# Kernel optimization log

Hardware: AMD Instinct MI355X
Metric: run time of the kernel (lower is better)

Reference implementation:

```python
import jax, jax.numpy as jnp
import numpy as np

B, T, H, S = 2, 2048, 16, 64
EMB = H * S  # 1024


def layer_norm(x, g, b, eps=1e-5):
    mu = jnp.mean(x, axis=-1, keepdims=True)
    var = jnp.var(x, axis=-1, keepdims=True)
    return (x - mu) * jax.lax.rsqrt(var + eps) * g + b


def setup_inputs() -> dict:
    key = jax.random.key(0)
    ks = jax.random.split(key, 12)
    sc = 0.02
    return {
        "x": jax.random.normal(ks[0], (B, T, EMB), dtype=jnp.float32),
        "Wkqv": jax.random.normal(ks[1], (S, 3 * S), dtype=jnp.float32) * sc,
        "Wproj": jax.random.normal(ks[2], (EMB, EMB), dtype=jnp.float32) * sc,
        "g1": jnp.ones((EMB,), jnp.float32),
        "b1": jnp.zeros((EMB,), jnp.float32),
        "W1": jax.random.normal(ks[3], (EMB, 4 * EMB), dtype=jnp.float32) * sc,
        "bff1": jnp.zeros((4 * EMB,), jnp.float32),
        "W2": jax.random.normal(ks[4], (4 * EMB, EMB), dtype=jnp.float32) * sc,
        "bff2": jnp.zeros((EMB,), jnp.float32),
        "g2": jnp.ones((EMB,), jnp.float32),
        "b2": jnp.zeros((EMB,), jnp.float32),
    }


def reference(x, Wkqv, Wproj, g1, b1, W1, bff1, W2, bff2, g2, b2):
    Bb, Tt, _ = x.shape
    xh = x.reshape(Bb, Tt, H, S)                     # [B,T,H,S]
    kqv = jnp.einsum('bths,sd->bthd', xh, Wkqv)      # [B,T,H,3S], shared per-head weight
    k, q, v = jnp.split(kqv, 3, axis=-1)             # note order: k, q, v
    scores = jnp.einsum('bihk,bjhk->bijh', q, k) / jnp.sqrt(jnp.float32(S))
    att = jax.nn.softmax(scores, axis=2)             # softmax over key dim j
    res = jnp.einsum('btih,bihs->bths', att, v).reshape(Bb, Tt, EMB)
    mha = res @ Wproj                                # Linear(emb, emb, bias=False)
    x = layer_norm(x + mha, g1, b1)
    h = jax.nn.gelu(x @ W1 + bff1, approximate=False)
    ff = h @ W2 + bff2
    return layer_norm(x + ff, g2, b2)
```

## Files before the change

### kernel.cpp

```cpp
#include <hip/hip_runtime.h>
#include <hip/hip_bf16.h>
#include <math.h>

#define B_ 2
#define T_ 2048
#define H_ 16
#define S_ 64
#define EMB 1024
#define FF 4096
#define BT (B_*T_)
#define ROWS (B_*T_*H_)

typedef __attribute__((ext_vector_type(8))) short s16x8;
typedef __attribute__((ext_vector_type(4))) float f32x4;

struct P4 { unsigned short* p[4]; };

__device__ __forceinline__ unsigned short f2b(float f) {
    return __builtin_bit_cast(unsigned short, __float2bfloat16(f));
}
__device__ __forceinline__ float b2f(short u) {
    return __builtin_bit_cast(float, ((unsigned int)(unsigned short)u) << 16);
}

__device__ __forceinline__ void gl_lds16(const void* g, void* l) {
    __builtin_amdgcn_global_load_lds(
        (const __attribute__((address_space(1))) void*)g,
        (__attribute__((address_space(3))) void*)l, 16, 0, 0);
}

__device__ __forceinline__ f32x4 mfma16(s16x8 a, s16x8 b, f32x4 c) {
    return __builtin_amdgcn_mfma_f32_16x16x32_bf16(a, b, c, 0, 0, 0);
}

#define WAIT_VM8 0x0F78
#define WAIT_VM2 0x0F72
#define WAIT_VM0 0x0F70

__global__ __launch_bounds__(256) void kqv_kernel(const float* __restrict__ x,
        const unsigned short* __restrict__ Wqt, unsigned short* __restrict__ K,
        unsigned short* __restrict__ Q, unsigned short* __restrict__ V) {
    const int tid = threadIdx.x;
    const int w = tid >> 6, lane = tid & 63;
    const int l15 = lane & 15, quad = lane >> 4;
    const long r0 = (long)blockIdx.x * 128 + w * 32;

    s16x8 af[2][2];
    #pragma unroll
    for (int mt = 0; mt < 2; ++mt)
        #pragma unroll
        for (int ks = 0; ks < 2; ++ks) {
            const float* xp = x + (r0 + mt*16 + l15) * 64 + ks*32 + quad*8;
            const float4 v0 = *(const float4*)xp;
            const float4 v1 = *(const float4*)(xp + 4);
            s16x8 a;
            a[0] = (short)f2b(v0.x); a[1] = (short)f2b(v0.y);
            a[2] = (short)f2b(v0.z); a[3] = (short)f2b(v0.w);
            a[4] = (short)f2b(v1.x); a[5] = (short)f2b(v1.y);
            a[6] = (short)f2b(v1.z); a[7] = (short)f2b(v1.w);
            af[mt][ks] = a;
        }

    #pragma unroll
    for (int nt = 0; nt < 12; ++nt) {
        const s16x8 b0 = *(const s16x8*)&Wqt[(nt*16 + l15)*64 + quad*8];
        const s16x8 b1 = *(const s16x8*)&Wqt[(nt*16 + l15)*64 + 32 + quad*8];
        f32x4 acc[2] = {};
        #pragma unroll
        for (int mt = 0; mt < 2; ++mt) {
            acc[mt] = mfma16(af[mt][0], b0, acc[mt]);
            acc[mt] = mfma16(af[mt][1], b1, acc[mt]);
        }
        unsigned short* dst = (nt < 4) ? K : (nt < 8) ? Q : V;
        const int c0 = (nt & 3) * 16 + l15;
        #pragma unroll
        for (int mt = 0; mt < 2; ++mt)
            #pragma unroll
            for (int r = 0; r < 4; ++r)
                dst[(r0 + mt*16 + quad*4 + r) * 64 + c0] = f2b(acc[mt][r]);
    }
}

__global__ __launch_bounds__(256) void vt_kernel(const unsigned short* __restrict__ V,
        unsigned short* __restrict__ VT) {
    __shared__ unsigned short Ts[64][72];
    const int tid = threadIdx.x;
    const int tt = blockIdx.x, bh = blockIdx.y;
    const int b = bh >> 4, h = bh & 15;
    const long vbase = ((long)b * (T_*H_) + h) * 64;
    #pragma unroll
    for (int i = 0; i < 2; ++i) {
        const int id = i * 256 + tid;
        const int tr = id >> 3, dc = (id & 7) * 8;
        const s16x8 v = *(const s16x8*)&V[vbase + (long)(tt*64 + tr)*1024 + dc];
        *(s16x8*)&Ts[tr][dc] = v;
    }
    __syncthreads();
    #pragma unroll
    for (int i = 0; i < 2; ++i) {
        const int id = i * 256 + tid;
        const int d = id >> 3, tc = (id & 7) * 8;
        s16x8 o;
        #pragma unroll
        for (int j = 0; j < 8; ++j) o[j] = (short)Ts[tc + j][d];
        *(s16x8*)&VT[((long)bh*64 + d)*2048 + tt*64 + tc] = o;
    }
}

__global__ __launch_bounds__(256) void attn_kernel(const unsigned short* __restrict__ Q,
        const unsigned short* __restrict__ K, const unsigned short* __restrict__ VT,
        unsigned short* __restrict__ res) {
    __shared__ __align__(16) unsigned short Kbuf[2][2][32*32];
    __shared__ __align__(16) unsigned short Vbuf[2][64*32];
    __shared__ __align__(16) unsigned short Ps[4][32*36];
    const int tid = threadIdx.x;
    const int wid = tid >> 6, lane = tid & 63;
    const int l15 = lane & 15, quad = lane >> 4;
    const int bid = blockIdx.x;
    const int qg = bid & 15, bh = bid >> 4;
    const int b = bh >> 4, h = bh & 15;
    const long base = ((long)b * (T_*H_) + h) * 64;
    const unsigned short* Qp = Q + base;
    const unsigned short* Kp = K + base;
    const unsigned short* Vp = VT + (long)bh * 64 * 2048;
    const int q0 = qg * 128 + wid * 32;
    unsigned short* ps = &Ps[wid][0];

    s16x8 qf[2][2];
    #pragma unroll
    for (int qq = 0; qq < 2; ++qq)
        #pragma unroll
        for (int ks = 0; ks < 2; ++ks) {
            const s16x8 raw = *(const s16x8*)&Qp[(long)(q0 + qq*16 + l15)*1024 + ks*32 + quad*8];
            s16x8 q;
            #pragma unroll
            for (int j = 0; j < 8; ++j) q[j] = (short)f2b(b2f(raw[j]) * 0.125f);
            qf[qq][ks] = q;
        }

    s16x8 onef;
    #pragma unroll
    for (int j = 0; j < 8; ++j) onef[j] = (short)0x3F80;

    f32x4 oacc[2][4] = {};
    f32x4 lacc[2] = {};

    const int j16 = lane >> 2;
    const int c8  = (lane & 3) * 8;

    auto stage = [&](int bufi, int kt) {
        char* kl = (char*)&Kbuf[bufi][0][0];
        char* vl = (char*)&Vbuf[bufi][0];
        const unsigned short* kg = Kp + (long)(kt*32) * 1024;
        const unsigned short* vg = Vp + kt*32 + c8;
        switch (wid) {
        case 0:
            gl_lds16(kg + (long)j16*1024 + c8,           kl +    0 + lane*16);
            gl_lds16(kg + (long)(j16+16)*1024 + c8,      kl + 1024 + lane*16);
            break;
        case 1:
            gl_lds16(kg + (long)j16*1024 + 32 + c8,      kl + 2048 + lane*16);
            gl_lds16(kg + (long)(j16+16)*1024 + 32 + c8, kl + 3072 + lane*16);
            break;
        case 2:
            gl_lds16(vg + (long)(j16     )*2048, vl +    0 + lane*16);
            gl_lds16(vg + (long)(j16 + 16)*2048, vl + 1024 + lane*16);
            break;
        default:
            gl_lds16(vg + (long)(j16 + 32)*2048, vl + 2048 + lane*16);
            gl_lds16(vg + (long)(j16 + 48)*2048, vl + 3072 + lane*16);
            break;
        }
    };

    auto compute = [&](int bufi) {
        f32x4 sT[2][2] = {};
        #pragma unroll
        for (int ks = 0; ks < 2; ++ks)
            #pragma unroll
            for (int jt = 0; jt < 2; ++jt) {
                const s16x8 kf = *(const s16x8*)&Kbuf[bufi][ks][(jt*16 + l15)*32 + quad*8];
                sT[jt][0] = mfma16(kf, qf[0][ks], sT[jt][0]);
                sT[jt][1] = mfma16(kf, qf[1][ks], sT[jt][1]);
            }
        #pragma unroll
        for (int jt = 0; jt < 2; ++jt)
            #pragma unroll
            for (int qq = 0; qq < 2; ++qq) {
                uint2 pk;
                pk.x = (unsigned int)f2b(__expf(sT[jt][qq][0]))
                     | ((unsigned int)f2b(__expf(sT[jt][qq][1])) << 16);
                pk.y = (unsigned int)f2b(__expf(sT[jt][qq][2]))
                     | ((unsigned int)f2b(__expf(sT[jt][qq][3])) << 16);
                *(uint2*)&ps[(qq*16 + l15)*36 + jt*16 + quad*4] = pk;
            }
        s16x8 pf[2];
        #pragma unroll
        for (int qq = 0; qq < 2; ++qq) {
            pf[qq] = *(const s16x8*)&ps[(qq*16 + l15)*36 + quad*8];
            lacc[qq] = mfma16(pf[qq], onef, lacc[qq]);
        }
        #pragma unroll
        for (int nt = 0; nt < 4; ++nt) {
            const s16x8 vf = *(const s16x8*)&Vbuf[bufi][(nt*16 + l15)*32 + quad*8];
            oacc[0][nt] = mfma16(pf[0], vf, oacc[0][nt]);
            oacc[1][nt] = mfma16(pf[1], vf, oacc[1][nt]);
        }
    };

    stage(0, 0);
    for (int kt = 0; kt < 63; ++kt) {
        stage((kt + 1) & 1, kt + 1);
        __builtin_amdgcn_s_waitcnt(WAIT_VM2);
        __builtin_amdgcn_s_barrier();
        __builtin_amdgcn_sched_barrier(0);
        compute(kt & 1);
        __builtin_amdgcn_s_barrier();
        __builtin_amdgcn_sched_barrier(0);
    }
    __builtin_amdgcn_s_waitcnt(WAIT_VM0);
    __builtin_amdgcn_s_barrier();
    __builtin_amdgcn_sched_barrier(0);
    compute(1);

    #pragma unroll
    for (int qq = 0; qq < 2; ++qq)
        #pragma unroll
        for (int r = 0; r < 4; ++r) {
            const float inv = 1.f / lacc[qq][r];
            const int t = q0 + qq*16 + quad*4 + r;
            #pragma unroll
            for (int nt = 0; nt < 4; ++nt)
                res[((long)(b*T_ + t))*EMB + h*64 + nt*16 + l15] =
                    f2b(oacc[qq][nt][r] * inv);
        }
}

__global__ __launch_bounds__(256) void gemm_gelu(const unsigned short* __restrict__ A,
        const unsigned short* __restrict__ Bt, const float* __restrict__ bias,
        unsigned short* __restrict__ C, int M, int N, int Kd) {
    __shared__ __align__(16) unsigned short As[2][128 * 32];
    __shared__ __align__(16) unsigned short Bs[2][128 * 32];
    const int tid = threadIdx.x;
    const int w = tid >> 6, lane = tid & 63;
    const int l15 = lane & 15, quad = lane >> 4;
    const int wm = w >> 1, wn = w & 1;
    const int bn = blockIdx.x, bm = blockIdx.y;
    const int sr = lane >> 2, skq = lane & 3;
    f32x4 acc[4][4] = {};
    const long arow = (long)(bm*128 + w*32 + sr);
    const long brow = (long)(bn*128 + w*32 + sr);

    auto stage = [&](int bi, int kt) {
        char* as = (char*)&As[bi][0];
        char* bs = (char*)&Bs[bi][0];
        gl_lds16(A  + (arow     )*Kd + kt + skq*8, as + (w*32     )*64 + lane*16);
        gl_lds16(A  + (arow + 16)*Kd + kt + skq*8, as + (w*32 + 16)*64 + lane*16);
        gl_lds16(Bt + (brow     )*Kd + kt + skq*8, bs + (w*32     )*64 + lane*16);
        gl_lds16(Bt + (brow + 16)*Kd + kt + skq*8, bs + (w*32 + 16)*64 + lane*16);
    };

    const int NT = Kd >> 5;
    stage(0, 0);
    __syncthreads();
    int bi = 0;
    for (int t = 0; t < NT; ++t) {
        if (t + 1 < NT) stage(bi ^ 1, (t + 1) * 32);
        s16x8 af[4], bf[4];
        #pragma unroll
        for (int mt = 0; mt < 4; ++mt)
            af[mt] = *(const s16x8*)&As[bi][(wm*64 + mt*16 + l15)*32 + quad*8];
        #pragma unroll
        for (int nt = 0; nt < 4; ++nt)
            bf[nt] = *(const s16x8*)&Bs[bi][(wn*64 + nt*16 + l15)*32 + quad*8];
        #pragma unroll
        for (int mt = 0; mt < 4; ++mt)
            #pragma unroll
            for (int nt = 0; nt < 4; ++nt)
                acc[mt][nt] = mfma16(af[mt], bf[nt], acc[mt][nt]);
        __syncthreads();
        bi ^= 1;
    }

    #pragma unroll
    for (int mt = 0; mt < 4; ++mt) {
        const int row0 = bm*128 + wm*64 + mt*16 + quad*4;
        #pragma unroll
        for (int nt = 0; nt < 4; ++nt) {
            const int col = bn*128 + wn*64 + nt*16 + l15;
            const float bv = bias[col];
            #pragma unroll
            for (int r = 0; r < 4; ++r) {
                float v = acc[mt][nt][r] + bv;
                v = 0.5f * v * (1.f + erff(v * 0.70710678118654752440f));
                C[(long)(row0 + r)*N + col] = f2b(v);
            }
        }
    }
}

__global__ __launch_bounds__(256) void gemm_splitk(const unsigned short* __restrict__ A,
        const unsigned short* __restrict__ Bt, P4 parts, int M, int N, int Kd, int Ks) {
    __shared__ __align__(16) unsigned short As[2][128 * 32];
    __shared__ __align__(16) unsigned short Bs[2][128 * 32];
    const int tid = threadIdx.x;
    const int w = tid >> 6, lane = tid & 63;
    const int l15 = lane & 15, quad = lane >> 4;
    const int wm = w >> 1, wn = w & 1;
    const int bn = blockIdx.x, bm = blockIdx.y, s = blockIdx.z;
    const int sr = lane >> 2, skq = lane & 3;
    f32x4 acc[4][4] = {};
    const long arow = (long)(bm*128 + w*32 + sr);
    const long brow = (long)(bn*128 + w*32 + sr);
    const int k0 = s * Ks;

    auto stage = [&](int bi, int kt) {
        char* as = (char*)&As[bi][0];
        char* bs = (char*)&Bs[bi][0];
        gl_lds16(A  + (arow     )*Kd + kt + skq*8, as + (w*32     )*64 + lane*16);
        gl_lds16(A  + (arow + 16)*Kd + kt + skq*8, as + (w*32 + 16)*64 + lane*16);
        gl_lds16(Bt + (brow     )*Kd + kt + skq*8, bs + (w*32     )*64 + lane*16);
        gl_lds16(Bt + (brow + 16)*Kd + kt + skq*8, bs + (w*32 + 16)*64 + lane*16);
    };

    const int NT = Ks >> 5;
    stage(0, k0);
    __syncthreads();
    int bi = 0;
    for (int t = 0; t < NT; ++t) {
        if (t + 1 < NT) stage(bi ^ 1, k0 + (t + 1) * 32);
        s16x8 af[4], bf[4];
        #pragma unroll
        for (int mt = 0; mt < 4; ++mt)
            af[mt] = *(const s16x8*)&As[bi][(wm*64 + mt*16 + l15)*32 + quad*8];
        #pragma unroll
        for (int nt = 0; nt < 4; ++nt)
            bf[nt] = *(const s16x8*)&Bs[bi][(wn*64 + nt*16 + l15)*32 + quad*8];
        #pragma unroll
        for (int mt = 0; mt < 4; ++mt)
            #pragma unroll
            for (int nt = 0; nt < 4; ++nt)
                acc[mt][nt] = mfma16(af[mt], bf[nt], acc[mt][nt]);
        __syncthreads();
        bi ^= 1;
    }

    unsigned short* Cp = parts.p[s];
    #pragma unroll
    for (int mt = 0; mt < 4; ++mt) {
        const int row0 = bm*128 + wm*64 + mt*16 + quad*4;
        #pragma unroll
        for (int nt = 0; nt < 4; ++nt) {
            const int col = bn*128 + wn*64 + nt*16 + l15;
            #pragma unroll
            for (int r = 0; r < 4; ++r)
                Cp[(long)(row0 + r)*N + col] = f2b(acc[mt][nt][r]);
        }
    }
}

template <int P, int XBF>
__global__ __launch_bounds__(256) void ln_kernel(const void* __restrict__ xa,
        P4 parts, const float* __restrict__ addb, const float* __restrict__ g,
        const float* __restrict__ bia, float* __restrict__ out,
        unsigned short* __restrict__ outb) {
    const int row = blockIdx.x;
    const int tid = threadIdx.x;
    float4 v;
    if (XBF) {
        const ushort4 u = ((const ushort4*)xa)[(long)row * (EMB/4) + tid];
        v.x = b2f((short)u.x); v.y = b2f((short)u.y);
        v.z = b2f((short)u.z); v.w = b2f((short)u.w);
    } else {
        v = ((const float4*)xa)[(long)row * (EMB/4) + tid];
    }
    #pragma unroll
    for (int p = 0; p < P; ++p) {
        const ushort4 u = ((const ushort4*)(parts.p[p] + (long)row * EMB))[tid];
        v.x += b2f((short)u.x); v.y += b2f((short)u.y);
        v.z += b2f((short)u.z); v.w += b2f((short)u.w);
    }
    if (addb) {
        const float4 ab = ((const float4*)addb)[tid];
        v.x += ab.x; v.y += ab.y; v.z += ab.z; v.w += ab.w;
    }
    float s = v.x + v.y + v.z + v.w;
    float ss = v.x * v.x + v.y * v.y + v.z * v.z + v.w * v.w;
    #pragma unroll
    for (int off = 32; off > 0; off >>= 1) {
        s += __shfl_down(s, off, 64);
        ss += __shfl_down(ss, off, 64);
    }
    __shared__ float ls[4], lss[4];
    __shared__ float mean_s, rstd_s;
    const int wid = tid >> 6, lane = tid & 63;
    if (lane == 0) { ls[wid] = s; lss[wid] = ss; }
    __syncthreads();
    if (tid == 0) {
        const float S0 = ls[0] + ls[1] + ls[2] + ls[3];
        const float S2 = lss[0] + lss[1] + lss[2] + lss[3];
        const float mean = S0 * (1.f / EMB);
        const float var = S2 * (1.f / EMB) - mean * mean;
        mean_s = mean;
        rstd_s = rsqrtf(var + 1e-5f);
    }
    __syncthreads();
    const float mean = mean_s, rstd = rstd_s;
    const float4 gg = ((const float4*)g)[tid];
    const float4 bb = ((const float4*)bia)[tid];
    float4 o;
    o.x = (v.x - mean) * rstd * gg.x + bb.x;
    o.y = (v.y - mean) * rstd * gg.y + bb.y;
    o.z = (v.z - mean) * rstd * gg.z + bb.z;
    o.w = (v.w - mean) * rstd * gg.w + bb.w;
    if (out) ((float4*)(out + (long)row * EMB))[tid] = o;
    if (outb) {
        unsigned short* ob = outb + (long)row * EMB + tid * 4;
        ob[0] = f2b(o.x); ob[1] = f2b(o.y); ob[2] = f2b(o.z); ob[3] = f2b(o.w);
    }
}

__global__ __launch_bounds__(256) void transp_all(const float* __restrict__ Wp,
        const float* __restrict__ W1, const float* __restrict__ W2,
        const float* __restrict__ Wq, unsigned short* __restrict__ Wpt,
        unsigned short* __restrict__ W1t, unsigned short* __restrict__ W2t,
        unsigned short* __restrict__ Wqt) {
    int id = blockIdx.x;
    const float* W; unsigned short* Wt; int Kd, N, ntx;
    if (id < 1024)      {            W = Wp; Wt = Wpt; Kd = 1024; N = 1024; ntx = 32; }
    else if (id < 5120) { id -= 1024; W = W1; Wt = W1t; Kd = 1024; N = 4096; ntx = 128; }
    else if (id < 9216) { id -= 5120; W = W2; Wt = W2t; Kd = 4096; N = 1024; ntx = 32; }
    else                { id -= 9216; W = Wq; Wt = Wqt; Kd = 64;   N = 192;  ntx = 6;  }
    __shared__ float Ts[32][33];
    const int tid = threadIdx.x;
    const int n0 = (id % ntx) * 32, k0 = (id / ntx) * 32;
    const int r = tid >> 3, c4 = (tid & 7) * 4;
    const float4 v = *(const float4*)&W[(long)(k0 + r) * N + n0 + c4];
    Ts[r][c4] = v.x; Ts[r][c4 + 1] = v.y; Ts[r][c4 + 2] = v.z; Ts[r][c4 + 3] = v.w;
    __syncthreads();
    #pragma unroll
    for (int i = 0; i < 4; ++i)
        Wt[(long)(n0 + r) * Kd + k0 + c4 + i] = f2b(Ts[c4 + i][r]);
}

extern "C" void kernel_launch(void* const* d_in, const int* in_sizes, int n_in,
                              void* d_out, int out_size, void* d_ws, size_t ws_size,
                              hipStream_t stream) {
    (void)in_sizes; (void)n_in; (void)out_size;
    const float* x     = (const float*)d_in[0];
    const float* Wkqv  = (const float*)d_in[1];
    const float* Wproj = (const float*)d_in[2];
    const float* g1    = (const float*)d_in[3];
    const float* b1    = (const float*)d_in[4];
    const float* W1    = (const float*)d_in[5];
    const float* bff1  = (const float*)d_in[6];
    const float* W2    = (const float*)d_in[7];
    const float* bff2  = (const float*)d_in[8];
    const float* g2    = (const float*)d_in[9];
    const float* b2    = (const float*)d_in[10];
    float* out = (float*)d_out;
    char* ws = (char*)d_ws;

    const size_t MB = 1u << 20;
    unsigned short* Qb   = (unsigned short*)(ws + 0 * MB);
    unsigned short* Kb   = (unsigned short*)(ws + 8 * MB);
    unsigned short* Vb   = (unsigned short*)(ws + 16 * MB);
    unsigned short* resb = (unsigned short*)(ws + 24 * MB);
    unsigned short* hb   = (unsigned short*)(ws + 8 * MB);
    unsigned short* VTb  = (unsigned short*)(ws + 40 * MB);
    unsigned short* mp0  = (unsigned short*)(ws + 40 * MB);
    unsigned short* mp1  = (unsigned short*)(ws + 48 * MB);
    unsigned short* x1b  = Qb;
    unsigned short* Wpt  = (unsigned short*)(ws + 72 * MB);
    unsigned short* W1t  = (unsigned short*)(ws + 74 * MB);
    unsigned short* W2t  = (unsigned short*)(ws + 82 * MB);
    unsigned short* Wqt  = (unsigned short*)(ws + 90 * MB);
    unsigned short* fp2  = (unsigned short*)(ws + 91 * MB);
    unsigned short* fp3  = (unsigned short*)(ws + 99 * MB);
    const bool big = ws_size >= 108 * MB;

    transp_all<<<dim3(9228), 256, 0, stream>>>(Wproj, W1, W2, Wkqv, Wpt, W1t, W2t, Wqt);

    kqv_kernel<<<dim3(ROWS/128), 256, 0, stream>>>(x, Wqt, Kb, Qb, Vb);
    vt_kernel<<<dim3(T_/64, B_*H_), 256, 0, stream>>>(Vb, VTb);
    attn_kernel<<<dim3(512), 256, 0, stream>>>(Qb, Kb, VTb, resb);
    P4 mp; mp.p[0] = mp0; mp.p[1] = mp1; mp.p[2] = nullptr; mp.p[3] = nullptr;
    gemm_splitk<<<dim3(EMB/128, BT/128, 2), 256, 0, stream>>>(resb, Wpt, mp, BT, EMB, EMB, EMB/2);
    ln_kernel<2, 0><<<dim3(BT), 256, 0, stream>>>(x, mp, nullptr, g1, b1, nullptr, x1b);
    gemm_gelu<<<dim3(FF/128, BT/128), 256, 0, stream>>>(x1b, W1t, bff1, hb, BT, FF, EMB);
    if (big) {
        P4 fp; fp.p[0] = mp0; fp.p[1] = mp1; fp.p[2] = fp2; fp.p[3] = fp3;
        gemm_splitk<<<dim3(EMB/128, BT/128, 4), 256, 0, stream>>>(hb, W2t, fp, BT, EMB, FF, FF/4);
        ln_kernel<4, 1><<<dim3(BT), 256, 0, stream>>>(x1b, fp, bff2, g2, b2, out, nullptr);
    } else {
        P4 fp; fp.p[0] = mp0; fp.p[1] = mp1; fp.p[2] = nullptr; fp.p[3] = nullptr;
        gemm_splitk<<<dim3(EMB/128, BT/128, 2), 256, 0, stream>>>(hb, W2t, fp, BT, EMB, FF, FF/2);
        ln_kernel<2, 1><<<dim3(BT), 256, 0, stream>>>(x1b, fp, bff2, g2, b2, out, nullptr);
    }
}
```

Before: 362.7 us.

## Split attention over key range into two partitions with a combine kernel

Result: no change. 358.7 us (-1.1%).

```diff
diff --git a/kernel.cpp b/kernel.cpp
--- a/kernel.cpp
+++ b/kernel.cpp
@@ -109,7 +109,7 @@
 
 __global__ __launch_bounds__(256) void attn_kernel(const unsigned short* __restrict__ Q,
         const unsigned short* __restrict__ K, const unsigned short* __restrict__ VT,
-        unsigned short* __restrict__ res) {
+        unsigned short* __restrict__ Op, float* __restrict__ lp) {
     __shared__ __align__(16) unsigned short Kbuf[2][2][32*32];
     __shared__ __align__(16) unsigned short Vbuf[2][64*32];
     __shared__ __align__(16) unsigned short Ps[4][32*36];
@@ -117,13 +117,14 @@
     const int wid = tid >> 6, lane = tid & 63;
     const int l15 = lane & 15, quad = lane >> 4;
     const int bid = blockIdx.x;
+    const int s = blockIdx.y;
     const int qg = bid & 15, bh = bid >> 4;
-    const int b = bh >> 4, h = bh & 15;
-    const long base = ((long)b * (T_*H_) + h) * 64;
+    const long base = ((long)(bh >> 4) * (T_*H_) + (bh & 15)) * 64;
     const unsigned short* Qp = Q + base;
     const unsigned short* Kp = K + base;
     const unsigned short* Vp = VT + (long)bh * 64 * 2048;
     const int q0 = qg * 128 + wid * 32;
+    const int kt0 = s * 32;
     unsigned short* ps = &Ps[wid][0];
 
     s16x8 qf[2][2];
@@ -208,9 +209,9 @@
         }
     };
 
-    stage(0, 0);
-    for (int kt = 0; kt < 63; ++kt) {
-        stage((kt + 1) & 1, kt + 1);
+    stage(0, kt0);
+    for (int kt = 0; kt < 31; ++kt) {
+        stage((kt + 1) & 1, kt0 + kt + 1);
         __builtin_amdgcn_s_waitcnt(WAIT_VM2);
         __builtin_amdgcn_s_barrier();
         __builtin_amdgcn_sched_barrier(0);
@@ -223,17 +224,35 @@
     __builtin_amdgcn_sched_barrier(0);
     compute(1);
 
+    unsigned short* op = Op + ((long)s * 32 + bh) * 2048 * 64;
+    float* lrow = lp + ((long)s * 32 + bh) * 2048;
     #pragma unroll
     for (int qq = 0; qq < 2; ++qq)
         #pragma unroll
         for (int r = 0; r < 4; ++r) {
-            const float inv = 1.f / lacc[qq][r];
             const int t = q0 + qq*16 + quad*4 + r;
+            if (l15 == 0) lrow[t] = lacc[qq][r];
             #pragma unroll
             for (int nt = 0; nt < 4; ++nt)
-                res[((long)(b*T_ + t))*EMB + h*64 + nt*16 + l15] =
-                    f2b(oacc[qq][nt][r] * inv);
-        }
+                op[(long)t*64 + nt*16 + l15] = f2b(oacc[qq][nt][r]);
+        }
+}
+
+__global__ __launch_bounds__(256) void attn_combine(const unsigned short* __restrict__ Op,
+        const float* __restrict__ lp, unsigned short* __restrict__ res) {
+    const int gid = blockIdx.x * 256 + threadIdx.x;
+    const int row = gid >> 4;
+    const int c4 = (gid & 15) * 4;
+    const int bh = row >> 11, t = row & 2047;
+    const int b = bh >> 4, h = bh & 15;
+    const float inv = 1.f / (lp[row] + lp[ROWS + row]);
+    const ushort4 u0 = *(const ushort4*)&Op[(long)row * 64 + c4];
+    const ushort4 u1 = *(const ushort4*)&Op[((long)ROWS + row) * 64 + c4];
+    unsigned short* r = res + ((long)(b*T_ + t)) * EMB + h*64 + c4;
+    r[0] = f2b((b2f((short)u0.x) + b2f((short)u1.x)) * inv);
+    r[1] = f2b((b2f((short)u0.y) + b2f((short)u1.y)) * inv);
+    r[2] = f2b((b2f((short)u0.z) + b2f((short)u1.z)) * inv);
+    r[3] = f2b((b2f((short)u0.w) + b2f((short)u1.w)) * inv);
 }
 
 __global__ __launch_bounds__(256) void gemm_gelu(const unsigned short* __restrict__ A,
@@ -470,6 +489,8 @@
     unsigned short* VTb  = (unsigned short*)(ws + 40 * MB);
     unsigned short* mp0  = (unsigned short*)(ws + 40 * MB);
     unsigned short* mp1  = (unsigned short*)(ws + 48 * MB);
+    unsigned short* Opb  = (unsigned short*)(ws + 48 * MB);
+    float*          lpb  = (float*)         (ws + 64 * MB);
     unsigned short* x1b  = Qb;
     unsigned short* Wpt  = (unsigned short*)(ws + 72 * MB);
     unsigned short* W1t  = (unsigned short*)(ws + 74 * MB);
@@ -483,7 +504,8 @@
 
     kqv_kernel<<<dim3(ROWS/128), 256, 0, stream>>>(x, Wqt, Kb, Qb, Vb);
     vt_kernel<<<dim3(T_/64, B_*H_), 256, 0, stream>>>(Vb, VTb);
-    attn_kernel<<<dim3(512), 256, 0, stream>>>(Qb, Kb, VTb, resb);
+    attn_kernel<<<dim3(512, 2), 256, 0, stream>>>(Qb, Kb, VTb, Opb, lpb);
+    attn_combine<<<dim3(ROWS*16/256), 256, 0, stream>>>(Opb, lpb, resb);
     P4 mp; mp.p[0] = mp0; mp.p[1] = mp1; mp.p[2] = nullptr; mp.p[3] = nullptr;
     gemm_splitk<<<dim3(EMB/128, BT/128, 2), 256, 0, stream>>>(resb, Wpt, mp, BT, EMB, EMB, EMB/2);
     ln_kernel<2, 0><<<dim3(BT), 256, 0, stream>>>(x, mp, nullptr, g1, b1, nullptr, x1b);
```
